# Performance work log

Measured on AMD Instinct MI355X. Metric: run time of the kernel, lower is better.

The kernel has to match this reference:

```python
import jax, jax.numpy as jnp
import numpy as np

DIM = 192
HEADS = 6
HD = 56            # inverted head dim: int((DIM//HEADS) * 1.75)
WIN = 7
N = WIN * WIN      # 49 tokens per window
NW = 64            # windows per image (56x56 map, 7x7 windows)
B_ = 2048          # num_windows * batch
SCALE = (DIM // HEADS) ** (-0.5)  # scale uses ORIGINAL head_dim=32


def _rel_index():
    # same construction as the torch buffer relative_position_index
    coords = np.stack(np.meshgrid(np.arange(WIN), np.arange(WIN), indexing='ij'))
    flat = coords.reshape(2, -1)                      # (2, N)
    rel = flat[:, :, None] - flat[:, None, :]          # (2, N, N)
    rel = rel.transpose(1, 2, 0).astype(np.int64)      # (N, N, 2)
    rel[..., 0] += WIN - 1
    rel[..., 1] += WIN - 1
    rel[..., 0] *= 2 * WIN - 1
    return jnp.asarray(rel.sum(-1), dtype=jnp.int32)   # (N, N)


def setup_inputs() -> dict:
    key = jax.random.key(0)
    ks = jax.random.split(key, 6)
    qkv_out = HEADS * HD * 3  # 1008
    return {
        'x': jax.random.normal(ks[0], (B_, N, DIM), jnp.float32),
        'mask': jnp.zeros((NW, N, N), jnp.float32),
        'qkv_w': (jax.random.normal(ks[1], (DIM, qkv_out), jnp.float32) * 0.02),
        'qkv_b': jnp.zeros((qkv_out,), jnp.float32),
        'rel_bias_table': (jax.random.normal(ks[2], ((2 * WIN - 1) ** 2, HEADS), jnp.float32) * 0.02),
        'rel_index': _rel_index(),
        'lepe_w': (jax.random.normal(ks[3], (HEADS * HD, 1, 3, 3), jnp.float32) * 0.02),
        'lepe_b': jnp.zeros((HEADS * HD,), jnp.float32),
        'proj_w': (jax.random.normal(ks[4], (HEADS * HD, DIM), jnp.float32) * 0.02),
        'proj_b': jnp.zeros((DIM,), jnp.float32),
    }


def reference(x, mask, qkv_w, qkv_b, rel_bias_table, rel_index, lepe_w, lepe_b, proj_w, proj_b):
    B, n, C = x.shape
    # qkv projection: (B, N, 3*H*HD) -> (B, H, N, 3*HD)
    qkv = (x @ qkv_w + qkv_b).reshape(B, n, HEADS, 3 * HD).transpose(0, 2, 1, 3)
    q, k, v = qkv[..., :HD], qkv[..., HD:2 * HD], qkv[..., 2 * HD:]

    v_img = v.transpose(0, 1, 3, 2).reshape(B, HEADS * HD, WIN, WIN)
    lepe = jax.lax.conv_general_dilated(
        v_img, lepe_w, window_strides=(1, 1), padding='SAME',
        dimension_numbers=('NCHW', 'OIHW', 'NCHW'),
        feature_group_count=HEADS * HD) + lepe_b[None, :, None, None]
    lepe = lepe.reshape(B, HEADS * HD, n).transpose(0, 2, 1)  # (B, N, H*HD)

    # attention scores + relative position bias + mask
    attn = jnp.einsum('bhnd,bhmd->bhnm', q * SCALE, k)
    bias = rel_bias_table[rel_index.reshape(-1)].reshape(n, n, HEADS).transpose(2, 0, 1)
    attn = attn + bias[None]
    nW = mask.shape[0]
    attn = attn.reshape(B // nW, nW, HEADS, n, n) + mask[None, :, None]
    attn = jax.nn.softmax(attn.reshape(B, HEADS, n, n), axis=-1)

    out = jnp.einsum('bhnm,bhmd->bhnd', attn, v)
    out = out.transpose(0, 2, 1, 3).reshape(B, n, HEADS * HD) + lepe
    return out @ proj_w + proj_b
```

## Files before the change

### kernel.cpp

```cpp
#include <hip/hip_runtime.h>
#include <hip/hip_bf16.h>

typedef __bf16 bf16x8 __attribute__((ext_vector_type(8)));
typedef unsigned short u16x8 __attribute__((ext_vector_type(8)));
typedef float f32x4 __attribute__((ext_vector_type(4)));

#define NTOK 49
#define NH   6
#define HDIM 56
#define DIMC 192
#define SCALE 0.17677669529663687f

#define WS_QKVWT   0u
#define WS_PROJWT  387072u
#define WS_QKVBS   522240u
#define WS_BMALLT  526272u
#define WS_LEPET   3672000u
#define WS_QKV     3684288u
#define WS_NEED    (WS_QKV + (size_t)100352 * 2016 + 4096)
#define FB_QKVWT  0
#define FB_PROJWT 387072
#define FB_BIAS6  534528

__device__ __forceinline__ unsigned swzaddr(unsigned base, int row, int colb, int strideb) {
  return base + (unsigned)((row * strideb + colb) ^ ((row & 7) << 4));
}

__device__ __forceinline__ unsigned short f2bu(float f) {
  __hip_bfloat16 h = __float2bfloat16(f);
  unsigned short u;
  __builtin_memcpy(&u, &h, 2);
  return u;
}

__device__ __forceinline__ float bu2f(unsigned short u) {
  union { unsigned int i; float f; } x;
  x.i = ((unsigned int)u) << 16;
  return x.f;
}


__global__ void prep_main(const float* __restrict__ qkv_w,
                          const float* __restrict__ qkv_b,
                          const float* __restrict__ proj_w,
                          const float* __restrict__ tbl,
                          const int* __restrict__ ridx,
                          const float* __restrict__ mask,
                          const float* __restrict__ lepe_w,
                          unsigned char* __restrict__ ws) {
  __hip_bfloat16* qkvwt   = (__hip_bfloat16*)(ws + WS_QKVWT);
  __hip_bfloat16* projwt2 = (__hip_bfloat16*)(ws + WS_PROJWT);
  float*          qkvbs   = (float*)(ws + WS_QKVBS);
  __hip_bfloat16* bmallT  = (__hip_bfloat16*)(ws + WS_BMALLT);
  float*          lepeT   = (float*)(ws + WS_LEPET);
  int idx = blockIdx.x * 256 + threadIdx.x;
  const int n1 = 1008 * 192;
  const int n2 = 192 * 352;
  const int n3 = 1008;
  const int n4 = 64 * 6 * 64 * 64;
  const int n5 = 9 * 336;
  if (idx < n1) {
    int c = idx / 192, k = idx - c * 192;
    float v = qkv_w[k * 1008 + c];
    if (c % 168 < 56) v *= SCALE;
    qkvwt[idx] = __float2bfloat16(v);
  } else if (idx < n1 + n2) {
    int j = idx - n1;
    int n = j / 352, kk = j - n * 352;
    projwt2[j] = __float2bfloat16(kk < 336 ? proj_w[kk * 192 + n] : 0.0f);
  } else if (idx < n1 + n2 + n3) {
    int c = idx - n1 - n2;
    float v = qkv_b[c];
    if (c % 168 < 56) v *= SCALE;
    qkvbs[c] = v;
  } else if (idx < n1 + n2 + n3 + n4) {
    int j = idx - n1 - n2 - n3;
    int wh = j >> 12;
    int e = j & 4095;
    int n = e >> 6, m = e & 63;
    int wdx = wh / 6, h = wh - wdx * 6;
    float v;
    if (n >= NTOK) v = -1e30f;
    else if (m >= NTOK) v = 0.0f;
    else v = tbl[ridx[m * NTOK + n] * NH + h] + mask[wdx * (NTOK * NTOK) + m * NTOK + n];
    bmallT[j] = __float2bfloat16(v);
  } else if (idx < n1 + n2 + n3 + n4 + n5) {
    int j = idx - n1 - n2 - n3 - n4;
    int tap = j / 336, hd = j - tap * 336;
    lepeT[j] = lepe_w[hd * 9 + tap];
  }
}

__global__ __launch_bounds__(256, 2) void qkv_gemm(
    const float* __restrict__ x, unsigned char* __restrict__ ws) {
  __shared__ uint4 smem4[2560];
  unsigned char* sm = (unsigned char*)smem4;
  const __hip_bfloat16* qkvwt = (const __hip_bfloat16*)(ws + WS_QKVWT);
  const float* qkvbs = (const float*)(ws + WS_QKVBS);
  unsigned char* qkvbuf = ws + WS_QKV;

  const int tid = threadIdx.x;
  const int lane = tid & 63, wv = tid >> 6;
  const int l15 = lane & 15, l4 = lane >> 4;
  const int b = blockIdx.x;
  const int j = (b & 7) * 686 + (b >> 3);
  const int nbase = (j % 7) * 144;
  const int mbase = (j / 7) * 128;

  bf16x8 afr[2][6];
#pragma unroll
  for (int mt = 0; mt < 2; ++mt) {
    int g = mbase + wv * 32 + mt * 16 + l15;
    const float* xr = x + (size_t)g * DIMC;
#pragma unroll
    for (int kt = 0; kt < 6; ++kt) {
      const float4* p = (const float4*)(xr + kt * 32 + l4 * 8);
      float4 a = p[0], bb = p[1];
      union { unsigned short u[8]; bf16x8 v; } pk;
      pk.u[0] = f2bu(a.x); pk.u[1] = f2bu(a.y); pk.u[2] = f2bu(a.z); pk.u[3] = f2bu(a.w);
      pk.u[4] = f2bu(bb.x); pk.u[5] = f2bu(bb.y); pk.u[6] = f2bu(bb.z); pk.u[7] = f2bu(bb.w);
      afr[mt][kt] = pk.v;
    }
  }

  f32x4 acc[2][9];
#pragma unroll
  for (int nt = 0; nt < 9; ++nt) {
    float bb = qkvbs[nbase + nt * 16 + l15];
    acc[0][nt] = (f32x4){bb, bb, bb, bb};
    acc[1][nt] = (f32x4){bb, bb, bb, bb};
  }

#pragma unroll
  for (int kh = 0; kh < 2; ++kh) {
    if (kh) __syncthreads();
    for (int jj = tid; jj < 1728; jj += 256) {
      int row = jj / 12, c16 = jj - row * 12;
      uint4 v = *(const uint4*)((const unsigned char*)qkvwt +
                                (size_t)(nbase + row) * 384 + kh * 192 + c16 * 16);
      *(uint4*)(sm + swzaddr(0, row, c16 * 16, 256)) = v;
    }
    __syncthreads();
#pragma unroll
    for (int kt2 = 0; kt2 < 3; ++kt2) {
      const int kt = kh * 3 + kt2;
#pragma unroll
      for (int nt = 0; nt < 9; ++nt) {
        bf16x8 bf = *(const bf16x8*)(sm + swzaddr(0, nt * 16 + l15, kt2 * 64 + l4 * 16, 256));
        acc[0][nt] = __builtin_amdgcn_mfma_f32_16x16x32_bf16(afr[0][kt], bf, acc[0][nt], 0, 0, 0);
        acc[1][nt] = __builtin_amdgcn_mfma_f32_16x16x32_bf16(afr[1][kt], bf, acc[1][nt], 0, 0, 0);
      }
    }
  }
  __syncthreads();

#pragma unroll
  for (int mt = 0; mt < 2; ++mt)
#pragma unroll
    for (int nt = 0; nt < 9; ++nt)
#pragma unroll
      for (int r = 0; r < 4; ++r) {
        int row = wv * 32 + mt * 16 + l4 * 4 + r;
        *(unsigned short*)(sm + swzaddr(0, row, (nt * 16 + l15) * 2, 320)) =
            f2bu(acc[mt][nt][r]);
      }
  __syncthreads();
  for (int jj = tid; jj < 2304; jj += 256) {
    int row = jj / 18, c16 = jj - row * 18;
    uint4 v = *(const uint4*)(sm + swzaddr(0, row, c16 * 16, 320));
    *(uint4*)(qkvbuf + (size_t)(mbase + row) * 2016 + nbase * 2 + c16 * 16) = v;
  }
}

#define A_KS   0u
#define A_VT   8192u
#define A_BMT  16384u
#define A_ATT  24576u
#define A_VS   32768u
#define A_SMEM 40960u

__global__ __launch_bounds__(256, 4) void attn_head(
    const float* __restrict__ lepe_b, unsigned char* __restrict__ ws) {
  __shared__ uint4 smem4[A_SMEM / 16];
  unsigned char* sm = (unsigned char*)smem4;
  const unsigned char* bmallT = ws + WS_BMALLT;
  const float* lepeT = (const float*)(ws + WS_LEPET);
  unsigned char* qkvbuf = ws + WS_QKV;

  const int tid = threadIdx.x;
  const int lane = tid & 63, wv = tid >> 6;
  const int l15 = lane & 15, l4 = lane >> 4;
  const int b = blockIdx.x;
  const int j = (b & 7) * 1536 + (b >> 3);
  const int h = j % 6;
  const int win = j / 6;
  const int wdx = win & 63;
  unsigned char* qbase = qkvbuf + (size_t)win * (NTOK * 2016);

  {
    uint4 z = {0u, 0u, 0u, 0u};
    for (int i = tid; i < 1024; i += 256) smem4[i] = z;
  }
  __syncthreads();

  for (int jj = tid; jj < 343; jj += 256) {
    int m = jj % 49, c = jj / 49;
    const unsigned char* row = qbase + (size_t)m * 2016 + h * 336;
    uint4 kv = *(const uint4*)(row + 112 + c * 16);
    *(uint4*)(sm + swzaddr(A_KS, m, c * 16, 128)) = kv;
    uint4 vv = *(const uint4*)(row + 224 + c * 16);
    *(uint4*)(sm + swzaddr(A_VS, m, c * 16, 128)) = vv;
    union { uint4 q; unsigned short u[8]; } pk; pk.q = vv;
#pragma unroll
    for (int e = 0; e < 8; ++e)
      *(unsigned short*)(sm + swzaddr(A_VT, c * 8 + e, m * 2, 128)) = pk.u[e];
  }
  {
    const uint4* src = (const uint4*)(bmallT + (size_t)(wdx * NH + h) * 8192);
    for (int jj = tid; jj < 512; jj += 256) {
      int n = jj >> 3, c = jj & 7;
      *(uint4*)(sm + swzaddr(A_BMT, n, c * 16, 128)) = src[jj];
    }
  }
  const int arow = wv * 16 + l15;
  const int xr = arow < NTOK ? arow : NTOK - 1;
  bf16x8 qa[2];
#pragma unroll
  for (int kt = 0; kt < 2; ++kt)
    qa[kt] = *(const bf16x8*)(qbase + (size_t)xr * 2016 + h * 336 + kt * 64 + l4 * 16);
  __syncthreads();

  const int mc0 = wv * 16 + l4 * 4;
  f32x4 sv[4];
#pragma unroll
  for (int nt = 0; nt < 4; ++nt) {
    int n = nt * 16 + l15;
    unsigned long long bm8 =
        *(const unsigned long long*)(sm + swzaddr(A_BMT, n, mc0 * 2, 128));
#pragma unroll
    for (int r = 0; r < 4; ++r)
      sv[nt][r] = bu2f((unsigned short)(bm8 >> (16 * r)));
#pragma unroll
    for (int kt = 0; kt < 2; ++kt) {
      bf16x8 kb = *(const bf16x8*)(sm + swzaddr(A_KS, n, kt * 64 + l4 * 16, 128));
      sv[nt] = __builtin_amdgcn_mfma_f32_16x16x32_bf16(qa[kt], kb, sv[nt], 0, 0, 0);
    }
  }

#pragma unroll
  for (int r = 0; r < 4; ++r) {
    float mx = fmaxf(fmaxf(sv[0][r], sv[1][r]), fmaxf(sv[2][r], sv[3][r]));
    mx = fmaxf(mx, __shfl_xor(mx, 1));
    mx = fmaxf(mx, __shfl_xor(mx, 2));
    mx = fmaxf(mx, __shfl_xor(mx, 4));
    mx = fmaxf(mx, __shfl_xor(mx, 8));
    float p0 = __expf(sv[0][r] - mx), p1 = __expf(sv[1][r] - mx);
    float p2 = __expf(sv[2][r] - mx), p3 = __expf(sv[3][r] - mx);
    float sum = p0 + p1 + p2 + p3;
    sum += __shfl_xor(sum, 1);
    sum += __shfl_xor(sum, 2);
    sum += __shfl_xor(sum, 4);
    sum += __shfl_xor(sum, 8);
    float rinv = 1.0f / sum;
    sv[0][r] = p0 * rinv; sv[1][r] = p1 * rinv; sv[2][r] = p2 * rinv; sv[3][r] = p3 * rinv;
  }
#pragma unroll
  for (int nt = 0; nt < 4; ++nt) {
    int n = nt * 16 + l15;
#pragma unroll
    for (int r = 0; r < 4; ++r) {
      int m = mc0 + r;
      if (m < NTOK)
        *(__hip_bfloat16*)(sm + swzaddr(A_ATT, m, n * 2, 128)) = __float2bfloat16(sv[nt][r]);
    }
  }

  bf16x8 pa[2];
#pragma unroll
  for (int kt = 0; kt < 2; ++kt)
    pa[kt] = *(const bf16x8*)(sm + swzaddr(A_ATT, arow, kt * 64 + l4 * 16, 128));
  f32x4 ov[4];
#pragma unroll
  for (int nt = 0; nt < 4; ++nt) {
    f32x4 a0 = (f32x4){0.f, 0.f, 0.f, 0.f};
#pragma unroll
    for (int kt = 0; kt < 2; ++kt) {
      bf16x8 vb = *(const bf16x8*)(sm + swzaddr(A_VT, nt * 16 + l15, kt * 64 + l4 * 16, 128));
      a0 = __builtin_amdgcn_mfma_f32_16x16x32_bf16(pa[kt], vb, a0, 0, 0, 0);
    }
    ov[nt] = a0;
  }

  __syncthreads();
#pragma unroll
  for (int nt = 0; nt < 4; ++nt) {
    int d = nt * 16 + l15;
#pragma unroll
    for (int r = 0; r < 4; ++r) {
      int m = mc0 + r;
      *(float*)(sm + swzaddr(0, m, d * 4, 256)) = ov[nt][r];
    }
  }
  __syncthreads();

  for (int jj = tid; jj < 343; jj += 256) {
    int m = jj % 49, c = jj / 49;
    int y = m / 7, x0 = m - y * 7;
    float4 o0 = *(const float4*)(sm + swzaddr(0, m, c * 32, 256));
    float4 o1 = *(const float4*)(sm + swzaddr(0, m, c * 32 + 16, 256));
    const float4* lb = (const float4*)(lepe_b + h * HDIM + c * 8);
    float4 b0 = lb[0], b1 = lb[1];
    float4 a0, a1;
    a0.x = o0.x + b0.x; a0.y = o0.y + b0.y; a0.z = o0.z + b0.z; a0.w = o0.w + b0.w;
    a1.x = o1.x + b1.x; a1.y = o1.y + b1.y; a1.z = o1.z + b1.z; a1.w = o1.w + b1.w;
#pragma unroll
    for (int dy = 0; dy < 3; ++dy) {
      int yy = y + dy - 1;
      if (yy < 0 || yy >= 7) continue;
#pragma unroll
      for (int dx = 0; dx < 3; ++dx) {
        int xx = x0 + dx - 1;
        if (xx < 0 || xx >= 7) continue;
        int mp = yy * 7 + xx;
        u16x8 vsv = *(const u16x8*)(sm + swzaddr(A_VS, mp, c * 16, 128));
        const float4* wr = (const float4*)(lepeT + (dy * 3 + dx) * 336 + h * HDIM + c * 8);
        float4 w0 = wr[0], w1 = wr[1];
        a0.x += w0.x * bu2f(vsv[0]); a0.y += w0.y * bu2f(vsv[1]);
        a0.z += w0.z * bu2f(vsv[2]); a0.w += w0.w * bu2f(vsv[3]);
        a1.x += w1.x * bu2f(vsv[4]); a1.y += w1.y * bu2f(vsv[5]);
        a1.z += w1.z * bu2f(vsv[6]); a1.w += w1.w * bu2f(vsv[7]);
      }
    }
    union { unsigned short u[8]; uint4 q; } st;
    st.u[0] = f2bu(a0.x); st.u[1] = f2bu(a0.y); st.u[2] = f2bu(a0.z); st.u[3] = f2bu(a0.w);
    st.u[4] = f2bu(a1.x); st.u[5] = f2bu(a1.y); st.u[6] = f2bu(a1.z); st.u[7] = f2bu(a1.w);
    *(uint4*)(qbase + (size_t)m * 2016 + h * 336 + c * 16) = st.q;
  }
}

__global__ __launch_bounds__(256, 3) void proj_gemm(
    const float* __restrict__ proj_b, unsigned char* __restrict__ ws,
    float* __restrict__ out) {
  __shared__ uint4 smem4[2816];
  unsigned char* sm = (unsigned char*)smem4;
  const unsigned char* projwt2 = ws + WS_PROJWT;
  const unsigned char* qkvbuf = ws + WS_QKV;

  const int tid = threadIdx.x;
  const int lane = tid & 63, wv = tid >> 6;
  const int l15 = lane & 15, l4 = lane >> 4;
  const int b = blockIdx.x;
  const int j = (b & 7) * 294 + (b >> 3);
  const int nbase = (j % 3) * 64;
  const int mbase = (j / 3) * 128;

  for (int jj = tid; jj < 2816; jj += 256) {
    int n = jj / 44, c = jj - n * 44;
    uint4 v = *(const uint4*)(projwt2 + (size_t)(nbase + n) * 704 + c * 16);
    *(uint4*)(sm + swzaddr(0, n, c * 16, 704)) = v;
  }
  f32x4 acc[2][4];
#pragma unroll
  for (int nt = 0; nt < 4; ++nt) {
    float bb = proj_b[nbase + nt * 16 + l15];
    acc[0][nt] = (f32x4){bb, bb, bb, bb};
    acc[1][nt] = (f32x4){bb, bb, bb, bb};
  }
  __syncthreads();

  for (int kt = 0; kt < 11; ++kt) {
    int ks = kt * 32 + l4 * 8;
    int hh = ks / 56;
    int rem = ks - hh * 56;
    unsigned aoff = (unsigned)(hh * 336 + rem * 2);
    bf16x8 af[2];
#pragma unroll
    for (int mt = 0; mt < 2; ++mt) {
      int row = mbase + wv * 32 + mt * 16 + l15;
      af[mt] = *(const bf16x8*)(qkvbuf + (size_t)row * 2016 + aoff);
    }
#pragma unroll
    for (int nt = 0; nt < 4; ++nt) {
      bf16x8 pb = *(const bf16x8*)(sm + swzaddr(0, nt * 16 + l15, (kt * 32 + l4 * 8) * 2, 704));
      acc[0][nt] = __builtin_amdgcn_mfma_f32_16x16x32_bf16(af[0], pb, acc[0][nt], 0, 0, 0);
      acc[1][nt] = __builtin_amdgcn_mfma_f32_16x16x32_bf16(af[1], pb, acc[1][nt], 0, 0, 0);
    }
  }
  __syncthreads();

#pragma unroll
  for (int mt = 0; mt < 2; ++mt)
#pragma unroll
    for (int nt = 0; nt < 4; ++nt)
#pragma unroll
      for (int r = 0; r < 4; ++r) {
        int m = wv * 32 + mt * 16 + l4 * 4 + r;
        *(float*)(sm + swzaddr(0, m, (nt * 16 + l15) * 4, 256)) = acc[mt][nt][r];
      }
  __syncthreads();
  for (int jj = tid; jj < 2048; jj += 256) {
    int row = jj >> 4, c = jj & 15;
    uint4 v = *(const uint4*)(sm + swzaddr(0, row, c * 16, 256));
    *(uint4*)((unsigned char*)out + (size_t)(mbase + row) * 768 + nbase * 4 + c * 16) = v;
  }
}


__global__ void prep_fb(const float* __restrict__ qkv_w,
                        const float* __restrict__ proj_w,
                        const float* __restrict__ tbl,
                        const int* __restrict__ ridx,
                        unsigned char* __restrict__ ws) {
  __hip_bfloat16* qkvwt  = (__hip_bfloat16*)(ws + FB_QKVWT);
  __hip_bfloat16* projwt = (__hip_bfloat16*)(ws + FB_PROJWT);
  float* bias6 = (float*)(ws + FB_BIAS6);
  int idx = blockIdx.x * 256 + threadIdx.x;
  const int n1 = 1008 * 192;
  const int n2 = 192 * 384;
  const int n3 = 6 * 49 * 49;
  if (idx < n1) {
    int c = idx / 192, k = idx - c * 192;
    qkvwt[idx] = __float2bfloat16(qkv_w[k * 1008 + c]);
  } else if (idx < n1 + n2) {
    int j = idx - n1;
    int c = j / 384, kk = j - c * 384;
    projwt[j] = __float2bfloat16(kk < 336 ? proj_w[kk * 192 + c] : 0.0f);
  } else if (idx < n1 + n2 + n3) {
    int j = idx - n1 - n2;
    int h = j / 2401, mn = j - h * 2401;
    bias6[j] = tbl[ridx[mn] * 6 + h];
  }
}

#define QS_OFF  0
#define KS_OFF  8192
#define VT_OFF  16384
#define ATT_OFF 24576
#define SMEM_BYTES 32768

__global__ __launch_bounds__(256, 4) void winattn_fb(
    const float* __restrict__ x, const float* __restrict__ mask,
    const float* __restrict__ qkv_b, const float* __restrict__ lepe_w,
    const float* __restrict__ lepe_b, const float* __restrict__ proj_b,
    const unsigned char* __restrict__ ws, float* __restrict__ out) {
  __shared__ uint4 smem4[SMEM_BYTES / 16];
  unsigned char* sm = (unsigned char*)smem4;
  const __hip_bfloat16* qkvwt  = (const __hip_bfloat16*)(ws + FB_QKVWT);
  const __hip_bfloat16* projwt = (const __hip_bfloat16*)(ws + FB_PROJWT);
  const float* bias6 = (const float*)(ws + FB_BIAS6);

  const int tid = threadIdx.x;
  const int lane = tid & 63, wv = tid >> 6;
  const int l15 = lane & 15, l4 = lane >> 4;
  const int blk = blockIdx.x;
  const int wdx = blk & 63;
  {
    uint4 z = {0u, 0u, 0u, 0u};
    for (int i = tid; i < SMEM_BYTES / 16; i += 256) smem4[i] = z;
  }
  const int arow = wv * 16 + l15;
  const float* xg = x + (size_t)blk * (NTOK * DIMC);
  const int xr = arow < NTOK ? arow : NTOK - 1;
  bf16x8 afr[6];
#pragma unroll
  for (int kt = 0; kt < 6; ++kt) {
    const float4* p = (const float4*)(xg + xr * DIMC + kt * 32 + l4 * 8);
    float4 a = p[0], b = p[1];
    union { unsigned short u[8]; bf16x8 v; } pk;
    pk.u[0] = f2bu(a.x); pk.u[1] = f2bu(a.y); pk.u[2] = f2bu(a.z); pk.u[3] = f2bu(a.w);
    pk.u[4] = f2bu(b.x); pk.u[5] = f2bu(b.y); pk.u[6] = f2bu(b.z); pk.u[7] = f2bu(b.w);
    afr[kt] = pk.v;
  }
  f32x4 pacc[12];
#pragma unroll
  for (int nt = 0; nt < 12; ++nt) {
    float pb = proj_b[nt * 16 + l15];
    pacc[nt] = (f32x4){pb, pb, pb, pb};
  }
  const float* maskw = mask + wdx * (NTOK * NTOK);
  __syncthreads();

  for (int h = 0; h < NH; ++h) {
    for (int i = tid; i < NTOK * NTOK; i += 256) {
      int row = i / NTOK, col = i - row * NTOK;
      *(unsigned short*)(sm + ATT_OFF + row * 128 + col * 2) =
          f2bu(bias6[h * (NTOK * NTOK) + i] + maskw[i]);
    }
#pragma unroll
    for (int nt = 0; nt < 11; ++nt) {
      int cl = nt * 16 + l15;
      int cg = h * 168 + cl; if (cg > 1007) cg = 1007;
      float bias = qkv_b[cg];
      f32x4 acc = (f32x4){bias, bias, bias, bias};
#pragma unroll
      for (int kt = 0; kt < 6; ++kt) {
        bf16x8 bf = *(const bf16x8*)(qkvwt + cg * DIMC + kt * 32 + l4 * 8);
        acc = __builtin_amdgcn_mfma_f32_16x16x32_bf16(afr[kt], bf, acc, 0, 0, 0);
      }
      if (cl < 168) {
#pragma unroll
        for (int r = 0; r < 4; ++r) {
          int m = wv * 16 + l4 * 4 + r;
          if (m < NTOK) {
            float vv = acc[r];
            if (cl < 56)
              *(__hip_bfloat16*)(sm + swzaddr(QS_OFF, m, cl * 2, 128)) = __float2bfloat16(vv);
            else if (cl < 112)
              *(__hip_bfloat16*)(sm + swzaddr(KS_OFF, m, (cl - 56) * 2, 128)) = __float2bfloat16(vv);
            else
              *(__hip_bfloat16*)(sm + swzaddr(VT_OFF, cl - 112, m * 2, 128)) = __float2bfloat16(vv);
          }
        }
      }
    }
    __syncthreads();
    bf16x8 qa[2];
#pragma unroll
    for (int kt = 0; kt < 2; ++kt)
      qa[kt] = *(const bf16x8*)(sm + swzaddr(QS_OFF, arow, (kt * 32 + l4 * 8) * 2, 128));
    f32x4 sv[4];
#pragma unroll
    for (int nt = 0; nt < 4; ++nt) {
      f32x4 acc = (f32x4){0.f, 0.f, 0.f, 0.f};
#pragma unroll
      for (int kt = 0; kt < 2; ++kt) {
        bf16x8 kb = *(const bf16x8*)(sm + swzaddr(KS_OFF, nt * 16 + l15, (kt * 32 + l4 * 8) * 2, 128));
        acc = __builtin_amdgcn_mfma_f32_16x16x32_bf16(qa[kt], kb, acc, 0, 0, 0);
      }
      sv[nt] = acc;
    }
#pragma unroll
    for (int nt = 0; nt < 4; ++nt) {
      int n = nt * 16 + l15;
#pragma unroll
      for (int r = 0; r < 4; ++r) {
        int m = wv * 16 + l4 * 4 + r;
        int mc = m < NTOK ? m : NTOK - 1;
        float vv;
        if (n < NTOK) {
          float add = __bfloat162float(
              *(const __hip_bfloat16*)(sm + ATT_OFF + mc * 128 + n * 2));
          vv = SCALE * sv[nt][r] + add;
        } else {
          vv = -1e30f;
        }
        sv[nt][r] = vv;
      }
    }
#pragma unroll
    for (int r = 0; r < 4; ++r) {
      float mx = fmaxf(fmaxf(sv[0][r], sv[1][r]), fmaxf(sv[2][r], sv[3][r]));
      mx = fmaxf(mx, __shfl_xor(mx, 1));
      mx = fmaxf(mx, __shfl_xor(mx, 2));
      mx = fmaxf(mx, __shfl_xor(mx, 4));
      mx = fmaxf(mx, __shfl_xor(mx, 8));
      float p0 = __expf(sv[0][r] - mx), p1 = __expf(sv[1][r] - mx);
      float p2 = __expf(sv[2][r] - mx), p3 = __expf(sv[3][r] - mx);
      float sum = p0 + p1 + p2 + p3;
      sum += __shfl_xor(sum, 1);
      sum += __shfl_xor(sum, 2);
      sum += __shfl_xor(sum, 4);
      sum += __shfl_xor(sum, 8);
      float rinv = 1.0f / sum;
      sv[0][r] = p0 * rinv; sv[1][r] = p1 * rinv; sv[2][r] = p2 * rinv; sv[3][r] = p3 * rinv;
    }
#pragma unroll
    for (int nt = 0; nt < 4; ++nt) {
      int n = nt * 16 + l15;
#pragma unroll
      for (int r = 0; r < 4; ++r) {
        int m = wv * 16 + l4 * 4 + r;
        if (m < NTOK)
          *(__hip_bfloat16*)(sm + swzaddr(ATT_OFF, m, n * 2, 128)) = __float2bfloat16(sv[nt][r]);
      }
    }
    bf16x8 pa[2];
#pragma unroll
    for (int kt = 0; kt < 2; ++kt)
      pa[kt] = *(const bf16x8*)(sm + swzaddr(ATT_OFF, arow, (kt * 32 + l4 * 8) * 2, 128));
    f32x4 ov[4];
#pragma unroll
    for (int nt = 0; nt < 4; ++nt) {
      f32x4 acc = (f32x4){0.f, 0.f, 0.f, 0.f};
#pragma unroll
      for (int kt = 0; kt < 2; ++kt) {
        bf16x8 vb = *(const bf16x8*)(sm + swzaddr(VT_OFF, nt * 16 + l15, (kt * 32 + l4 * 8) * 2, 128));
        acc = __builtin_amdgcn_mfma_f32_16x16x32_bf16(pa[kt], vb, acc, 0, 0, 0);
      }
      ov[nt] = acc;
    }
#pragma unroll
    for (int nt = 0; nt < 4; ++nt) {
      int d = nt * 16 + l15;
      if (d < HDIM) {
        const float* lw = lepe_w + (h * HDIM + d) * 9;
        float w9[9];
#pragma unroll
        for (int t9 = 0; t9 < 9; ++t9) w9[t9] = lw[t9];
        float lb = lepe_b[h * HDIM + d];
#pragma unroll
        for (int r = 0; r < 4; ++r) {
          int m = wv * 16 + l4 * 4 + r;
          if (m < NTOK) {
            int y = m / 7, x0 = m - y * 7;
            float lac = lb;
#pragma unroll
            for (int dy = 0; dy < 3; ++dy)
#pragma unroll
              for (int dx = 0; dx < 3; ++dx) {
                int yy = y + dy - 1, xx = x0 + dx - 1;
                if (yy >= 0 && yy < 7 && xx >= 0 && xx < 7) {
                  float vvv = __bfloat162float(
                      *(const __hip_bfloat16*)(sm + swzaddr(VT_OFF, d, (yy * 7 + xx) * 2, 128)));
                  lac += w9[dy * 3 + dx] * vvv;
                }
              }
            *(__hip_bfloat16*)(sm + swzaddr(QS_OFF, m, d * 2, 128)) =
                __float2bfloat16(ov[nt][r] + lac);
          }
        }
      }
    }
    bf16x8 oa[2];
#pragma unroll
    for (int kt = 0; kt < 2; ++kt)
      oa[kt] = *(const bf16x8*)(sm + swzaddr(QS_OFF, arow, (kt * 32 + l4 * 8) * 2, 128));
#pragma unroll
    for (int nt = 0; nt < 12; ++nt) {
#pragma unroll
      for (int kt = 0; kt < 2; ++kt) {
        bf16x8 pb = *(const bf16x8*)(projwt + (nt * 16 + l15) * 384 + h * HDIM + kt * 32 + l4 * 8);
        pacc[nt] = __builtin_amdgcn_mfma_f32_16x16x32_bf16(oa[kt], pb, pacc[nt], 0, 0, 0);
      }
    }
    __syncthreads();
  }
  float* og = out + (size_t)blk * (NTOK * DIMC);
#pragma unroll
  for (int nt = 0; nt < 12; ++nt) {
#pragma unroll
    for (int r = 0; r < 4; ++r) {
      int m = wv * 16 + l4 * 4 + r;
      if (m < NTOK) og[m * DIMC + nt * 16 + l15] = pacc[nt][r];
    }
  }
}


extern "C" void kernel_launch(void* const* d_in, const int* in_sizes, int n_in,
                              void* d_out, int out_size, void* d_ws, size_t ws_size,
                              hipStream_t stream) {
  const float* x      = (const float*)d_in[0];
  const float* mask   = (const float*)d_in[1];
  const float* qkv_w  = (const float*)d_in[2];
  const float* qkv_b  = (const float*)d_in[3];
  const float* tbl    = (const float*)d_in[4];
  const int*   ridx   = (const int*)d_in[5];
  const float* lepe_w = (const float*)d_in[6];
  const float* lepe_b = (const float*)d_in[7];
  const float* proj_w = (const float*)d_in[8];
  const float* proj_b = (const float*)d_in[9];
  unsigned char* ws = (unsigned char*)d_ws;
  float* out = (float*)d_out;

  if (ws_size >= WS_NEED) {
    const int n_prep = 1008 * 192 + 192 * 352 + 1008 + 64 * 6 * 64 * 64 + 9 * 336;
    prep_main<<<dim3((n_prep + 255) / 256), dim3(256), 0, stream>>>(
        qkv_w, qkv_b, proj_w, tbl, ridx, mask, lepe_w, ws);
    qkv_gemm<<<dim3(5488), dim3(256), 0, stream>>>(x, ws);
    attn_head<<<dim3(12288), dim3(256), 0, stream>>>(lepe_b, ws);
    proj_gemm<<<dim3(2352), dim3(256), 0, stream>>>(proj_b, ws, out);
  } else {
    prep_fb<<<dim3(1101), dim3(256), 0, stream>>>(qkv_w, proj_w, tbl, ridx, ws);
    winattn_fb<<<dim3(2048), dim3(256), 0, stream>>>(x, mask, qkv_b, lepe_w, lepe_b,
                                                     proj_b, ws, out);
  }
}
```

Before: 325.0 us.

## Pre-convert x to bf16 and use smaller-tile QKV GEMM reading bf16 input

Adds a separate kernel that converts the fp32 input x to bf16 in workspace, and a new QKV GEMM that reads bf16 A fragments directly from global memory with 64-row M tiles instead of 128. It stages the weight tile in LDS in two K halves. The goal is to halve the A-operand read traffic in the GEMM and raise the block count, at the cost of an extra launch and a full write-plus-read of x in bf16. The new path runs only when the workspace is large enough.

```diff
diff --git a/kernel.cpp b/kernel.cpp
--- a/kernel.cpp
+++ b/kernel.cpp
@@ -18,6 +18,8 @@
 #define WS_LEPET   3672000u
 #define WS_QKV     3684288u
 #define WS_NEED    (WS_QKV + (size_t)100352 * 2016 + 4096)
+#define WS_XBF     (WS_QKV + (size_t)100352 * 2016)
+#define WS_NEED2   (WS_XBF + (size_t)100352 * 384 + 4096)
 #define FB_QKVWT  0
 #define FB_PROJWT 387072
 #define FB_BIAS6  534528
@@ -91,6 +93,83 @@
   }
 }
 
+__global__ __launch_bounds__(256) void xcvt(const float* __restrict__ x,
+                                            unsigned char* __restrict__ ws) {
+  unsigned char* xbf = ws + WS_XBF;
+  int i = blockIdx.x * 256 + threadIdx.x;
+  if (i >= 2408448) return;
+  const float4* p = (const float4*)(x + (size_t)i * 8);
+  float4 a = p[0], b = p[1];
+  union { unsigned short u[8]; uint4 q; } pk;
+  pk.u[0] = f2bu(a.x); pk.u[1] = f2bu(a.y); pk.u[2] = f2bu(a.z); pk.u[3] = f2bu(a.w);
+  pk.u[4] = f2bu(b.x); pk.u[5] = f2bu(b.y); pk.u[6] = f2bu(b.z); pk.u[7] = f2bu(b.w);
+  *(uint4*)(xbf + (size_t)i * 16) = pk.q;
+}
+
+__global__ __launch_bounds__(256, 2) void qkv_gemm3(unsigned char* __restrict__ ws) {
+  __shared__ uint4 smem4[2304];
+  unsigned char* sm = (unsigned char*)smem4;
+  const __hip_bfloat16* qkvwt = (const __hip_bfloat16*)(ws + WS_QKVWT);
+  const float* qkvbs = (const float*)(ws + WS_QKVBS);
+  const unsigned char* xbf = ws + WS_XBF;
+  unsigned char* qkvbuf = ws + WS_QKV;
+
+  const int tid = threadIdx.x;
+  const int lane = tid & 63, wv = tid >> 6;
+  const int l15 = lane & 15, l4 = lane >> 4;
+  const int b = blockIdx.x;
+  const int j = (b & 7) * 1372 + (b >> 3);
+  const int nbase = (j % 7) * 144;
+  const int mbase = (j / 7) * 64;
+
+  f32x4 acc[9];
+#pragma unroll
+  for (int nt = 0; nt < 9; ++nt) {
+    float bb = qkvbs[nbase + nt * 16 + l15];
+    acc[nt] = (f32x4){bb, bb, bb, bb};
+  }
+  const unsigned char* xrow = xbf + (size_t)(mbase + wv * 16 + l15) * 384;
+
+#pragma unroll
+  for (int kh = 0; kh < 2; ++kh) {
+    if (kh) __syncthreads();
+    for (int jj = tid; jj < 1728; jj += 256) {
+      int row = jj / 12, c16 = jj - row * 12;
+      uint4 v = *(const uint4*)((const unsigned char*)qkvwt +
+                                (size_t)(nbase + row) * 384 + kh * 192 + c16 * 16);
+      *(uint4*)(sm + swzaddr(0, row, c16 * 16, 256)) = v;
+    }
+    bf16x8 afr[3];
+#pragma unroll
+    for (int kt2 = 0; kt2 < 3; ++kt2)
+      afr[kt2] = *(const bf16x8*)(xrow + (kh * 3 + kt2) * 64 + l4 * 16);
+    __syncthreads();
+#pragma unroll
+    for (int kt2 = 0; kt2 < 3; ++kt2) {
+#pragma unroll
+      for (int nt = 0; nt < 9; ++nt) {
+        bf16x8 bf = *(const bf16x8*)(sm + swzaddr(0, nt * 16 + l15, kt2 * 64 + l4 * 16, 256));
+        acc[nt] = __builtin_amdgcn_mfma_f32_16x16x32_bf16(afr[kt2], bf, acc[nt], 0, 0, 0);
+      }
+    }
+  }
+  __syncthreads();
+
+#pragma unroll
+  for (int nt = 0; nt < 9; ++nt)
+#pragma unroll
+    for (int r = 0; r < 4; ++r) {
+      int row = wv * 16 + l4 * 4 + r;
+      *(unsigned short*)(sm + swzaddr(0, row, (nt * 16 + l15) * 2, 320)) = f2bu(acc[nt][r]);
+    }
+  __syncthreads();
+  for (int jj = tid; jj < 1152; jj += 256) {
+    int row = jj / 18, c16 = jj - row * 18;
+    uint4 v = *(const uint4*)(sm + swzaddr(0, row, c16 * 16, 320));
+    *(uint4*)(qkvbuf + (size_t)(mbase + row) * 2016 + nbase * 2 + c16 * 16) = v;
+  }
+}
+
 __global__ __launch_bounds__(256, 2) void qkv_gemm(
     const float* __restrict__ x, unsigned char* __restrict__ ws) {
   __shared__ uint4 smem4[2560];
@@ -667,7 +746,12 @@
     const int n_prep = 1008 * 192 + 192 * 352 + 1008 + 64 * 6 * 64 * 64 + 9 * 336;
     prep_main<<<dim3((n_prep + 255) / 256), dim3(256), 0, stream>>>(
         qkv_w, qkv_b, proj_w, tbl, ridx, mask, lepe_w, ws);
-    qkv_gemm<<<dim3(5488), dim3(256), 0, stream>>>(x, ws);
+    if (ws_size >= WS_NEED2) {
+      xcvt<<<dim3(9408), dim3(256), 0, stream>>>(x, ws);
+      qkv_gemm3<<<dim3(10976), dim3(256), 0, stream>>>(ws);
+    } else {
+      qkv_gemm<<<dim3(5488), dim3(256), 0, stream>>>(x, ws);
+    }
     attn_head<<<dim3(12288), dim3(256), 0, stream>>>(lepe_b, ws);
     proj_gemm<<<dim3(2352), dim3(256), 0, stream>>>(proj_b, ws, out);
   } else {
```

Result: faster. 296.3 us (-8.8%).
